# Kernel tuning notes

Hardware: AMD Instinct MI355X
Metric: run time of the kernel (lower is better)

The kernel has to match this reference:

```python
import jax, jax.numpy as jnp
import numpy as np

N = 50000      # nodes
E = 500000     # directed edges
F_IN = 112     # node feature dim
G = 256        # number of graphs in batch


def _lin(key, fan_in, fan_out):
    # torch nn.Linear default init: U(-1/sqrt(fan_in), 1/sqrt(fan_in))
    s = 1.0 / np.sqrt(fan_in)
    kw, kb = jax.random.split(key)
    W = jax.random.uniform(kw, (fan_in, fan_out), jnp.float32, -s, s)
    b = jax.random.uniform(kb, (fan_out,), jnp.float32, -s, s)
    return W, b


def setup_inputs() -> dict:
    key = jax.random.key(0)
    ks = jax.random.split(key, 9)
    x = jax.random.normal(ks[0], (N, F_IN), jnp.float32)
    edge_index = jax.random.randint(ks[1], (2, E), 0, N)
    # sorted graph ids, guaranteeing every graph id 0..G-1 appears
    batch = jnp.sort(jnp.concatenate([jnp.arange(G),
                                      jax.random.randint(ks[2], (N - G,), 0, G)]))
    W1, b1 = _lin(ks[3], F_IN, 336)
    W2, b2 = _lin(ks[4], 336, 168)
    Wg, bg = _lin(ks[5], 168, 84)
    Wf, bf = _lin(ks[6], 84, 42)
    Wo, bo = _lin(ks[7], 42, 1)
    return dict(x=x, edge_index=edge_index, batch=batch,
                W1=W1, b1=b1, W2=W2, b2=b2,
                Wg=Wg, bg=bg, Wf=Wf, bf=bf, Wo=Wo, bo=bo)


def _gcn_conv(x, W, b, src, dst, n):
    """PyG GCNConv: add self-loops, symmetric D^-1/2 A D^-1/2 normalization."""
    h = x @ W                                   # [n, out]
    loop = jnp.arange(n, dtype=src.dtype)
    src_f = jnp.concatenate([src, loop])        # [E+n]
    dst_f = jnp.concatenate([dst, loop])
    deg = jax.ops.segment_sum(jnp.ones(src_f.shape[0], jnp.float32), dst_f, n)
    dinv = jnp.where(deg > 0, jax.lax.rsqrt(deg), 0.0)
    norm = dinv[src_f] * dinv[dst_f]            # [E+n]
    out = jax.ops.segment_sum(h[src_f] * norm[:, None], dst_f, n)
    return out + b


def reference(x, edge_index, batch, W1, b1, W2, b2, Wg, bg, Wf, bf, Wo, bo):
    src, dst = edge_index[0], edge_index[1]
    h = jax.nn.relu(_gcn_conv(x, W1, b1, src, dst, N))
    # dropout is identity in eval mode
    h = jax.nn.relu(_gcn_conv(h, W2, b2, src, dst, N))
    g = jax.ops.segment_max(h, batch, G)        # global max pool -> [G, 168]
    g = jax.nn.relu(g @ Wg + bg)
    g = jax.nn.relu(g @ Wf + bf)
    return g @ Wo + bo                           # [G, 1]
```

## Files before the change

kernel.cpp:

```cpp
#include <hip/hip_runtime.h>
#include <hip/hip_fp16.h>

#define N_NODES 50000
#define MPAD    50048
#define N_EDGES 500000
#define F_IN    112
#define K1X     112
#define K1P     128
#define F1      336
#define K2P     352
#define F2      168
#define NGRAPH  256

typedef __attribute__((ext_vector_type(8))) _Float16 f16x8;
typedef __attribute__((ext_vector_type(4))) float f32x4;
typedef unsigned short ushort_t;

__device__ __forceinline__ ushort_t f16_bits(float x) {
    __half h = __float2half_rn(x);
    return *(ushort_t*)&h;
}

__device__ __forceinline__ void gload_b64(uint2& d, const ushort_t* a) {
    asm volatile("global_load_dwordx2 %0, %1, off" : "=v"(d) : "v"(a));
}
__device__ __forceinline__ void gload_b128(uint4& d, const ushort_t* a) {
    asm volatile("global_load_dwordx4 %0, %1, off" : "=v"(d) : "v"(a));
}
__device__ __forceinline__ void vmwait0() {
    asm volatile("s_waitcnt vmcnt(0)" ::: "memory");
    __builtin_amdgcn_sched_barrier(0);
}

__global__ void k_zero_int(int* p, int n) {
    int i = blockIdx.x * blockDim.x + threadIdx.x;
    if (i < n) p[i] = 0;
}

#define CVX_ELEMS  (N_NODES * 28)
#define CVX_BLOCKS ((CVX_ELEMS + 255) / 256)
#define CNT_BLOCKS  ((N_EDGES / 2 + 255) / 256)
#define CVW1_BLOCKS ((384 * K1P + 255) / 256)
#define CVW2_BLOCKS ((192 * K2P + 255) / 256)
#define PREP_BLOCKS (CVX_BLOCKS + CNT_BLOCKS + CVW1_BLOCKS + CVW2_BLOCKS)

__global__ __launch_bounds__(256) void k_prep(const float* __restrict__ x,
                                              const int* __restrict__ dst,
                                              const float* __restrict__ W1,
                                              const float* __restrict__ W2,
                                              ushort_t* __restrict__ x16,
                                              int* __restrict__ dcount,
                                              ushort_t* __restrict__ w1t,
                                              ushort_t* __restrict__ w2t) {
    int bid = blockIdx.x;
    int t = threadIdx.x;
    if (bid < CVX_BLOCKS) {
        int i = bid * 256 + t;
        if (i < CVX_ELEMS) {
            float4 f = ((const float4*)x)[i];
            __half2 h0 = __floats2half2_rn(f.x, f.y);
            __half2 h1 = __floats2half2_rn(f.z, f.w);
            uint2 u; u.x = *(unsigned*)&h0; u.y = *(unsigned*)&h1;
            ((uint2*)x16)[i] = u;
        }
        return;
    }
    bid -= CVX_BLOCKS;
    if (bid < CNT_BLOCKS) {
        int i = bid * 256 + t;
        if (i < N_EDGES / 2) {
            int2 d = ((const int2*)dst)[i];
            atomicAdd(&dcount[d.x], 1);
            atomicAdd(&dcount[d.y], 1);
        }
        return;
    }
    bid -= CNT_BLOCKS;
    if (bid < CVW1_BLOCKS) {
        int idx = bid * 256 + t;
        if (idx < 384 * K1P) {
            int n = idx / K1P, k = idx % K1P;
            float v = (n < F1 && k < F_IN) ? W1[k * F1 + n] : 0.0f;
            w1t[idx] = f16_bits(v);
        }
        return;
    }
    bid -= CVW1_BLOCKS;
    {
        int idx = bid * 256 + t;
        if (idx < 192 * K2P) {
            int n = idx / K2P, k = idx % K2P;
            float v = (n < F2 && k < F1) ? W2[k * F2 + n] : 0.0f;
            w2t[idx] = f16_bits(v);
        }
    }
}

__global__ __launch_bounds__(256) void k_offsets(const int* __restrict__ dcount,
                                                 int* __restrict__ ctr,
                                                 int* __restrict__ off,
                                                 int* __restrict__ pend,
                                                 float* __restrict__ dinv) {
    int w = blockIdx.x * 256 + threadIdx.x;
    int lane = threadIdx.x & 63;
    bool valid = w < N_NODES / 2;
    int dA = valid ? dcount[2 * w] : 0;
    int dB = valid ? dcount[2 * w + 1] : 0;
    int tot = dA + dB;
    int pre = tot;
    #pragma unroll
    for (int d = 1; d < 64; d <<= 1) {
        int y = __shfl_up(pre, d);
        if (lane >= d) pre += y;
    }
    int wtotal = __shfl(pre, 63);
    int base = 0;
    if (lane == 0) base = atomicAdd(ctr, wtotal);
    base = __shfl(base, 0);
    int o0 = base + pre - tot;
    if (valid) {
        off[2 * w]     = o0;
        off[2 * w + 1] = o0 + dA;
        pend[w]        = o0 + tot;
        dinv[2 * w]     = rsqrtf((float)dA + 1.0f);
        dinv[2 * w + 1] = rsqrtf((float)dB + 1.0f);
    }
}

__global__ void k_scatter(const int* __restrict__ src, const int* __restrict__ dst,
                          const int* __restrict__ off, int* __restrict__ dcount,
                          const float* __restrict__ dinv,
                          int2* __restrict__ csr, int e2) {
    int i = blockIdx.x * blockDim.x + threadIdx.x;
    if (i >= e2) return;
    int2 s2 = ((const int2*)src)[i];
    int2 d2 = ((const int2*)dst)[i];
    {
        int pos = atomicSub(&dcount[d2.x], 1) - 1;
        int2 rec; rec.x = s2.x; rec.y = __float_as_int(dinv[s2.x] * dinv[d2.x]);
        csr[off[d2.x] + pos] = rec;
    }
    {
        int pos = atomicSub(&dcount[d2.y], 1) - 1;
        int2 rec; rec.x = s2.y; rec.y = __float_as_int(dinv[s2.y] * dinv[d2.y]);
        csr[off[d2.y] + pos] = rec;
    }
}

__global__ __launch_bounds__(256) void k_agg1(const ushort_t* __restrict__ X16,
                                              const int* __restrict__ off,
                                              const int* __restrict__ pend,
                                              const int2* __restrict__ csr,
                                              const float* __restrict__ dinv,
                                              ushort_t* __restrict__ aX) {
    int w = (blockIdx.x * 256 + threadIdx.x) >> 6;
    int lane = threadIdx.x & 63;
    if (w >= N_NODES / 2) return;
    const int g = lane >> 5, sl = lane & 31;
    const int slc = min(sl, 27);
    const int v = 2 * w + g;
    const bool act = sl < 28;
    int o0A = off[2 * w], oM = off[2 * w + 1], o1B = pend[w];
    int o0 = g ? oM : o0A;
    int n  = g ? (o1B - oM) : (oM - o0A);
    int nmax = max(oM - o0A, o1B - oM);
    int total = o1B - o0A;
    float di = dinv[v];
    float s2 = di * di;
    float4 acc;
    {
        uint2 us = *(const uint2*)(X16 + (long)v * K1X + slc * 4);
        float2 sf0 = __half22float2(*(__half2*)&us.x);
        float2 sf1 = __half22float2(*(__half2*)&us.y);
        acc.x = sf0.x * s2; acc.y = sf0.y * s2; acc.z = sf1.x * s2; acc.w = sf1.y * s2;
    }
    int nm1 = max(n - 1, 0);
    if (total <= 64) {
        int2 eall = csr[min(o0A + lane, N_EDGES - 1)];
        int ebase = o0 - o0A;
        for (int b = 0; b < nmax; b += 8) {
            int es[8]; float ec[8];
            #pragma unroll
            for (int j = 0; j < 8; ++j) {
                int widx = ebase + min(b + j, nm1);
                es[j] = __shfl(eall.x, widx);
                ec[j] = __int_as_float(__shfl(eall.y, widx));
            }
            uint2 u[8];
            #pragma unroll
            for (int j = 0; j < 8; ++j)
                gload_b64(u[j], X16 + (long)es[j] * K1X + slc * 4);
            vmwait0();
            #pragma unroll
            for (int j = 0; j < 8; ++j) {
                float c = ((b + j) < n) ? ec[j] : 0.0f;
                float2 f0 = __half22float2(*(__half2*)&u[j].x);
                float2 f1 = __half22float2(*(__half2*)&u[j].y);
                acc.x += c * f0.x; acc.y += c * f0.y; acc.z += c * f1.x; acc.w += c * f1.y;
            }
        }
    } else {
        for (int b = 0; b < nmax; b += 8) {
            int2 e[8];
            #pragma unroll
            for (int j = 0; j < 8; ++j) {
                int cidx = min(o0 + min(b + j, nm1), N_EDGES - 1);
                e[j] = csr[cidx];
            }
            uint2 u[8];
            #pragma unroll
            for (int j = 0; j < 8; ++j)
                gload_b64(u[j], X16 + (long)e[j].x * K1X + slc * 4);
            vmwait0();
            #pragma unroll
            for (int j = 0; j < 8; ++j) {
                float c = ((b + j) < n) ? __int_as_float(e[j].y) : 0.0f;
                float2 f0 = __half22float2(*(__half2*)&u[j].x);
                float2 f1 = __half22float2(*(__half2*)&u[j].y);
                acc.x += c * f0.x; acc.y += c * f0.y; acc.z += c * f1.x; acc.w += c * f1.y;
            }
        }
    }
    __half2 h0 = __floats2half2_rn(acc.x, acc.y);
    __half2 h1 = __floats2half2_rn(acc.z, acc.w);
    uint2 o; o.x = *(unsigned*)&h0; o.y = *(unsigned*)&h1;
    if (!act) { o.x = 0; o.y = 0; }
    *(uint2*)(aX + (long)v * K1P + sl * 4) = o;
}

__global__ __launch_bounds__(256) void k_gemm_fused(
        const ushort_t* __restrict__ aX,
        const ushort_t* __restrict__ w1t,
        const float* __restrict__ b1,
        const ushort_t* __restrict__ w2t,
        ushort_t* __restrict__ T2) {
    __shared__ ushort_t As[64][40];
    __shared__ ushort_t Bs[352][40];
    __shared__ ushort_t H1s[64][360];
    const int tid = threadIdx.x;
    const int row0 = blockIdx.x * 64;
    const int w = tid >> 6, l = tid & 63;
    const int wm = w >> 1, wn = w & 1;
    const int lm = l & 15, lq = l >> 4;

    f32x4 acc1[2][11];
    #pragma unroll
    for (int i = 0; i < 2; ++i)
        #pragma unroll
        for (int j = 0; j < 11; ++j) acc1[i][j] = (f32x4){0.f, 0.f, 0.f, 0.f};

    for (int k0 = 0; k0 < K1P; k0 += 32) {
        {
            int r = tid >> 2, s = (tid & 3) * 8;
            *(int4*)&As[r][s] = *(const int4*)&aX[(long)(row0 + r) * K1P + k0 + s];
        }
        #pragma unroll
        for (int it = 0; it < 6; ++it) {
            int f = tid + it * 256;
            if (f < 1408) {
                int r = f >> 2, s = (f & 3) * 8;
                *(int4*)&Bs[r][s] = *(const int4*)&w1t[(long)r * K1P + k0 + s];
            }
        }
        __syncthreads();
        f16x8 af0 = *(const f16x8*)&As[wm * 32 + lm][lq * 8];
        f16x8 af1 = *(const f16x8*)&As[wm * 32 + 16 + lm][lq * 8];
        #pragma unroll
        for (int ns = 0; ns < 11; ++ns) {
            f16x8 bf = *(const f16x8*)&Bs[wn * 176 + ns * 16 + lm][lq * 8];
            acc1[0][ns] = __builtin_amdgcn_mfma_f32_16x16x32_f16(af0, bf, acc1[0][ns], 0, 0, 0);
            acc1[1][ns] = __builtin_amdgcn_mfma_f32_16x16x32_f16(af1, bf, acc1[1][ns], 0, 0, 0);
        }
        __syncthreads();
    }
    #pragma unroll
    for (int ms = 0; ms < 2; ++ms)
        #pragma unroll
        for (int ns = 0; ns < 11; ++ns) {
            int col = wn * 176 + ns * 16 + lm;
            float bb = (col < F1) ? b1[col] : 0.0f;
            #pragma unroll
            for (int i = 0; i < 4; ++i) {
                int r = wm * 32 + ms * 16 + lq * 4 + i;
                H1s[r][col] = f16_bits(fmaxf(acc1[ms][ns][i] + bb, 0.0f));
            }
        }
    __syncthreads();

    f32x4 acc2[2][6];
    #pragma unroll
    for (int i = 0; i < 2; ++i)
        #pragma unroll
        for (int j = 0; j < 6; ++j) acc2[i][j] = (f32x4){0.f, 0.f, 0.f, 0.f};

    for (int k0 = 0; k0 < K2P; k0 += 32) {
        #pragma unroll
        for (int it = 0; it < 3; ++it) {
            int f = tid + it * 256;
            int r = f >> 2, s = (f & 3) * 8;
            *(int4*)&Bs[r][s] = *(const int4*)&w2t[(long)r * K2P + k0 + s];
        }
        __syncthreads();
        f16x8 af0 = *(const f16x8*)&H1s[wm * 32 + lm][k0 + lq * 8];
        f16x8 af1 = *(const f16x8*)&H1s[wm * 32 + 16 + lm][k0 + lq * 8];
        #pragma unroll
        for (int ns = 0; ns < 6; ++ns) {
            f16x8 bf = *(const f16x8*)&Bs[wn * 96 + ns * 16 + lm][lq * 8];
            acc2[0][ns] = __builtin_amdgcn_mfma_f32_16x16x32_f16(af0, bf, acc2[0][ns], 0, 0, 0);
            acc2[1][ns] = __builtin_amdgcn_mfma_f32_16x16x32_f16(af1, bf, acc2[1][ns], 0, 0, 0);
        }
        __syncthreads();
    }
    #pragma unroll
    for (int ms = 0; ms < 2; ++ms)
        #pragma unroll
        for (int ns = 0; ns < 6; ++ns) {
            int col = wn * 96 + ns * 16 + lm;
            if (col < F2) {
                #pragma unroll
                for (int i = 0; i < 4; ++i) {
                    int r = row0 + wm * 32 + ms * 16 + lq * 4 + i;
                    T2[(long)r * F2 + col] = f16_bits(acc2[ms][ns][i]);
                }
            }
        }
}

__global__ __launch_bounds__(256) void k_agg2(const ushort_t* __restrict__ T16,
                                              const int* __restrict__ off,
                                              const int* __restrict__ pend,
                                              const int2* __restrict__ csr,
                                              const float* __restrict__ dinv,
                                              const float* __restrict__ b2,
                                              const int* __restrict__ batch,
                                              float* __restrict__ gmax) {
    __shared__ __align__(16) float smax[8][168];
    __shared__ int sb[8];
    int tid = threadIdx.x;
    int w = (blockIdx.x * 256 + tid) >> 6;
    int lane = tid & 63;
    const int g = lane >> 5, sl = lane & 31;
    const int slc = min(sl, 20);
    const int nib = tid >> 5;
    const int v = 2 * w + g;
    const bool act = sl < 21;
    int o0A = off[2 * w], oM = off[2 * w + 1], o1B = pend[w];
    int o0 = g ? oM : o0A;
    int n  = g ? (o1B - oM) : (oM - o0A);
    int nmax = max(oM - o0A, o1B - oM);
    int total = o1B - o0A;
    float di = dinv[v];
    float4 a0, a1;
    {
        uint4 u = *(const uint4*)(T16 + (long)v * F2 + slc * 8);
        float2 f0 = __half22float2(*(__half2*)&u.x);
        float2 f1 = __half22float2(*(__half2*)&u.y);
        float2 f2 = __half22float2(*(__half2*)&u.z);
        float2 f3 = __half22float2(*(__half2*)&u.w);
        float s2 = di * di;
        a0.x = f0.x * s2; a0.y = f0.y * s2; a0.z = f1.x * s2; a0.w = f1.y * s2;
        a1.x = f2.x * s2; a1.y = f2.y * s2; a1.z = f3.x * s2; a1.w = f3.y * s2;
    }
    int nm1 = max(n - 1, 0);
    if (total <= 64) {
        int2 eall = csr[min(o0A + lane, N_EDGES - 1)];
        int ebase = o0 - o0A;
        for (int b = 0; b < nmax; b += 8) {
            int es[8]; float ec[8];
            #pragma unroll
            for (int j = 0; j < 8; ++j) {
                int widx = ebase + min(b + j, nm1);
                es[j] = __shfl(eall.x, widx);
                ec[j] = __int_as_float(__shfl(eall.y, widx));
            }
            uint4 u[8];
            #pragma unroll
            for (int j = 0; j < 8; ++j)
                gload_b128(u[j], T16 + (long)es[j] * F2 + slc * 8);
            vmwait0();
            #pragma unroll
            for (int j = 0; j < 8; ++j) {
                float c = ((b + j) < n) ? ec[j] : 0.0f;
                float2 f0 = __half22float2(*(__half2*)&u[j].x);
                float2 f1 = __half22float2(*(__half2*)&u[j].y);
                float2 f2 = __half22float2(*(__half2*)&u[j].z);
                float2 f3 = __half22float2(*(__half2*)&u[j].w);
                a0.x += c * f0.x; a0.y += c * f0.y; a0.z += c * f1.x; a0.w += c * f1.y;
                a1.x += c * f2.x; a1.y += c * f2.y; a1.z += c * f3.x; a1.w += c * f3.y;
            }
        }
    } else {
        for (int b = 0; b < nmax; b += 8) {
            int2 e[8];
            #pragma unroll
            for (int j = 0; j < 8; ++j) {
                int cidx = min(o0 + min(b + j, nm1), N_EDGES - 1);
                e[j] = csr[cidx];
            }
            uint4 u[8];
            #pragma unroll
            for (int j = 0; j < 8; ++j)
                gload_b128(u[j], T16 + (long)e[j].x * F2 + slc * 8);
            vmwait0();
            #pragma unroll
            for (int j = 0; j < 8; ++j) {
                float c = ((b + j) < n) ? __int_as_float(e[j].y) : 0.0f;
                float2 f0 = __half22float2(*(__half2*)&u[j].x);
                float2 f1 = __half22float2(*(__half2*)&u[j].y);
                float2 f2 = __half22float2(*(__half2*)&u[j].z);
                float2 f3 = __half22float2(*(__half2*)&u[j].w);
                a0.x += c * f0.x; a0.y += c * f0.y; a0.z += c * f1.x; a0.w += c * f1.y;
                a1.x += c * f2.x; a1.y += c * f2.y; a1.z += c * f3.x; a1.w += c * f3.y;
            }
        }
    }
    if (act) {
        float4 bb0 = ((const float4*)b2)[sl * 2];
        float4 bb1 = ((const float4*)b2)[sl * 2 + 1];
        a0.x = fmaxf(a0.x + bb0.x, 0.0f); a0.y = fmaxf(a0.y + bb0.y, 0.0f);
        a0.z = fmaxf(a0.z + bb0.z, 0.0f); a0.w = fmaxf(a0.w + bb0.w, 0.0f);
        a1.x = fmaxf(a1.x + bb1.x, 0.0f); a1.y = fmaxf(a1.y + bb1.y, 0.0f);
        a1.z = fmaxf(a1.z + bb1.z, 0.0f); a1.w = fmaxf(a1.w + bb1.w, 0.0f);
        ((float4*)&smax[nib][0])[sl * 2]     = a0;
        ((float4*)&smax[nib][0])[sl * 2 + 1] = a1;
    }
    if ((tid & 31) == 0) sb[nib] = batch[v];
    __syncthreads();
    if (tid < F2) {
        int f = tid;
        int bp = sb[0];
        float m = smax[0][f];
        #pragma unroll
        for (int r = 1; r < 8; ++r) {
            int bc = sb[r];
            float vv = smax[r][f];
            if (bc == bp) { m = fmaxf(m, vv); }
            else {
                atomicMax((int*)&gmax[bp * F2 + f], __float_as_int(m));
                m = vv; bp = bc;
            }
        }
        atomicMax((int*)&gmax[bp * F2 + f], __float_as_int(m));
    }
}

__global__ __launch_bounds__(128) void k_head(const float* __restrict__ gmax,
        const float* __restrict__ Wg, const float* __restrict__ bg,
        const float* __restrict__ Wf, const float* __restrict__ bf,
        const float* __restrict__ Wo, const float* __restrict__ bo,
        float* __restrict__ out) {
    __shared__ float s1[84];
    __shared__ float s2[42];
    int gi = blockIdx.x;
    const float* s0 = gmax + (long)gi * F2;
    int t = threadIdx.x;
    if (t < 84) {
        float acc = bg[t];
        #pragma unroll 4
        for (int k = 0; k < F2; ++k) acc += s0[k] * Wg[k * 84 + t];
        s1[t] = fmaxf(acc, 0.0f);
    }
    __syncthreads();
    if (t < 42) {
        float acc = bf[t];
        #pragma unroll 4
        for (int k = 0; k < 84; ++k) acc += s1[k] * Wf[k * 42 + t];
        s2[t] = fmaxf(acc, 0.0f);
    }
    __syncthreads();
    if (t == 0) {
        float acc = bo[0];
        for (int k = 0; k < 42; ++k) acc += s2[k] * Wo[k];
        out[gi] = acc;
    }
}

extern "C" void kernel_launch(void* const* d_in, const int* in_sizes, int n_in,
                              void* d_out, int out_size, void* d_ws, size_t ws_size,
                              hipStream_t stream) {
    const float* x   = (const float*)d_in[0];
    const int*   ei  = (const int*)d_in[1];
    const int*   bat = (const int*)d_in[2];
    const float* W1  = (const float*)d_in[3];
    const float* b1  = (const float*)d_in[4];
    const float* W2  = (const float*)d_in[5];
    const float* b2  = (const float*)d_in[6];
    const float* Wg  = (const float*)d_in[7];
    const float* bg  = (const float*)d_in[8];
    const float* Wf  = (const float*)d_in[9];
    const float* bf  = (const float*)d_in[10];
    const float* Wo  = (const float*)d_in[11];
    const float* bo  = (const float*)d_in[12];
    float* out = (float*)d_out;

    char* p = (char*)d_ws;
    float* dinv     = (float*)p; p += 50048 * 4;
    int*   dcount   = (int*)p;   p += 50048 * 4;
    float* gmax     = (float*)p; p += NGRAPH * F2 * 4;
    int*   ctr      = (int*)p;   p += 16 * 4;
    int*   off      = (int*)p;   p += 100096 * 4;
    int*   pend     = (int*)p;   p += 25024 * 4;
    int2*  csr      = (int2*)p;  p += (long)N_EDGES * 8;
    ushort_t* x16   = (ushort_t*)p; p += (long)N_NODES * K1X * 2;
    ushort_t* aX    = (ushort_t*)p; p += (long)MPAD * K1P * 2;
    ushort_t* w1t   = (ushort_t*)p; p += (long)384 * K1P * 2;
    ushort_t* w2t   = (ushort_t*)p; p += (long)192 * K2P * 2;
    ushort_t* t16   = (ushort_t*)p; p += (long)MPAD * F2 * 2;

    const int* src = ei;
    const int* dst = ei + N_EDGES;
    const int B = 256;
    const int ZERO_WORDS = 50048 + NGRAPH * F2 + 16;

    k_zero_int<<<(ZERO_WORDS + B - 1) / B, B, 0, stream>>>(dcount, ZERO_WORDS);
    k_prep<<<PREP_BLOCKS, B, 0, stream>>>(x, dst, W1, W2, x16, dcount, w1t, w2t);
    k_offsets<<<(N_NODES / 2 + B - 1) / B, B, 0, stream>>>(dcount, ctr, off, pend, dinv);
    k_scatter<<<(N_EDGES / 2 + B - 1) / B, B, 0, stream>>>(src, dst, off, dcount, dinv, csr, N_EDGES / 2);

    k_agg1<<<(N_NODES / 2 * 64) / 256, 256, 0, stream>>>(x16, off, pend, csr, dinv, aX);
    k_gemm_fused<<<MPAD / 64, 256, 0, stream>>>(aX, w1t, b1, w2t, t16);

    k_agg2<<<(N_NODES / 2 * 64) / 256, 256, 0, stream>>>(t16, off, pend, csr, dinv, b2, bat, gmax);

    k_head<<<NGRAPH, 128, 0, stream>>>(gmax, Wg, bg, Wf, bf, Wo, bo, out);
}
```

Before: 256.8 us.

## Read GEMM weight fragments directly from global and double-buffer the A tile

The fused two-layer GEMM kernel no longer stages the W1 and W2 tiles in shared memory. Each wave loads its MFMA B fragments straight from global memory, relying on the small weight matrices staying in cache. The input tile is double-buffered so the next K slice loads while the current one is consumed. The second GEMM loop drops all barriers and becomes fully unrolled. This removes large shared-memory staging writes and barriers per K step, at the cost of more uncoalesced global and L2 traffic for the weight reads.

```diff
diff --git a/kernel.cpp b/kernel.cpp
--- a/kernel.cpp
+++ b/kernel.cpp
@@ -234,14 +234,14 @@
         const float* __restrict__ b1,
         const ushort_t* __restrict__ w2t,
         ushort_t* __restrict__ T2) {
-    __shared__ ushort_t As[64][40];
-    __shared__ ushort_t Bs[352][40];
+    __shared__ ushort_t As[2][64][40];
     __shared__ ushort_t H1s[64][360];
     const int tid = threadIdx.x;
     const int row0 = blockIdx.x * 64;
     const int w = tid >> 6, l = tid & 63;
     const int wm = w >> 1, wn = w & 1;
     const int lm = l & 15, lq = l >> 4;
+    const int sr = tid >> 2, ss = (tid & 3) * 8;
 
     f32x4 acc1[2][11];
     #pragma unroll
@@ -249,25 +249,18 @@
         #pragma unroll
         for (int j = 0; j < 11; ++j) acc1[i][j] = (f32x4){0.f, 0.f, 0.f, 0.f};
 
-    for (int k0 = 0; k0 < K1P; k0 += 32) {
-        {
-            int r = tid >> 2, s = (tid & 3) * 8;
-            *(int4*)&As[r][s] = *(const int4*)&aX[(long)(row0 + r) * K1P + k0 + s];
-        }
-        #pragma unroll
-        for (int it = 0; it < 6; ++it) {
-            int f = tid + it * 256;
-            if (f < 1408) {
-                int r = f >> 2, s = (f & 3) * 8;
-                *(int4*)&Bs[r][s] = *(const int4*)&w1t[(long)r * K1P + k0 + s];
-            }
-        }
-        __syncthreads();
-        f16x8 af0 = *(const f16x8*)&As[wm * 32 + lm][lq * 8];
-        f16x8 af1 = *(const f16x8*)&As[wm * 32 + 16 + lm][lq * 8];
+    *(int4*)&As[0][sr][ss] = *(const int4*)&aX[(long)(row0 + sr) * K1P + ss];
+    __syncthreads();
+    #pragma unroll
+    for (int ks = 0; ks < 4; ++ks) {
+        const int k0 = ks * 32;
+        if (ks < 3)
+            *(int4*)&As[(ks + 1) & 1][sr][ss] = *(const int4*)&aX[(long)(row0 + sr) * K1P + k0 + 32 + ss];
+        f16x8 af0 = *(const f16x8*)&As[ks & 1][wm * 32 + lm][lq * 8];
+        f16x8 af1 = *(const f16x8*)&As[ks & 1][wm * 32 + 16 + lm][lq * 8];
         #pragma unroll
         for (int ns = 0; ns < 11; ++ns) {
-            f16x8 bf = *(const f16x8*)&Bs[wn * 176 + ns * 16 + lm][lq * 8];
+            f16x8 bf = *(const f16x8*)&w1t[(long)(wn * 176 + ns * 16 + lm) * K1P + k0 + lq * 8];
             acc1[0][ns] = __builtin_amdgcn_mfma_f32_16x16x32_f16(af0, bf, acc1[0][ns], 0, 0, 0);
             acc1[1][ns] = __builtin_amdgcn_mfma_f32_16x16x32_f16(af1, bf, acc1[1][ns], 0, 0, 0);
         }
@@ -293,23 +286,17 @@
         #pragma unroll
         for (int j = 0; j < 6; ++j) acc2[i][j] = (f32x4){0.f, 0.f, 0.f, 0.f};
 
-    for (int k0 = 0; k0 < K2P; k0 += 32) {
-        #pragma unroll
-        for (int it = 0; it < 3; ++it) {
-            int f = tid + it * 256;
-            int r = f >> 2, s = (f & 3) * 8;
-            *(int4*)&Bs[r][s] = *(const int4*)&w2t[(long)r * K2P + k0 + s];
-        }
-        __syncthreads();
+    #pragma unroll
+    for (int ks = 0; ks < 11; ++ks) {
+        const int k0 = ks * 32;
         f16x8 af0 = *(const f16x8*)&H1s[wm * 32 + lm][k0 + lq * 8];
         f16x8 af1 = *(const f16x8*)&H1s[wm * 32 + 16 + lm][k0 + lq * 8];
         #pragma unroll
         for (int ns = 0; ns < 6; ++ns) {
-            f16x8 bf = *(const f16x8*)&Bs[wn * 96 + ns * 16 + lm][lq * 8];
+            f16x8 bf = *(const f16x8*)&w2t[(long)(wn * 96 + ns * 16 + lm) * K2P + k0 + lq * 8];
             acc2[0][ns] = __builtin_amdgcn_mfma_f32_16x16x32_f16(af0, bf, acc2[0][ns], 0, 0, 0);
             acc2[1][ns] = __builtin_amdgcn_mfma_f32_16x16x32_f16(af1, bf, acc2[1][ns], 0, 0, 0);
         }
-        __syncthreads();
     }
     #pragma unroll
     for (int ms = 0; ms < 2; ++ms)
```

New measurement: 270.6 us. +5.4%, slower.
